# Performance work log

Measured on AMD Instinct MI355X. Metric: run time of the kernel, lower is better.

Reference implementation:

```python
import jax, jax.numpy as jnp
import numpy as np

INPUT_DIM = 1024
HIDDEN = [4096, 4096, 4096]
OUTPUT_DIM = 1024


def _cplx(a):
    # a: float32 array with leading axis 2 = (real, imag)
    return (a[0] + 1j * a[1]).astype(jnp.complex64)


def setup_inputs() -> dict:
    key = jax.random.key(0)
    ks = list(jax.random.split(key, 16))
    O = [INPUT_DIM] + HIDDEN[:-1] + [OUTPUT_DIM]  # O[0], O[1], O[2], O[3]
    I = HIDDEN  # I[1..3]
    inp = {"x": jax.random.normal(ks[0], (2, INPUT_DIM), dtype=jnp.float32)}
    for l in range(3):
        Il, Ol, Oprev = I[l], O[l + 1], O[l]
        w_std = 1.0 / np.sqrt(Il)
        c_std = 1.0 / np.sqrt(2 * Oprev)
        inp[f"W{l+1}"] = (jax.random.normal(ks[1 + 4 * l], (2, Ol, Il), dtype=jnp.float32) * w_std)
        inp[f"b{l+1}"] = jnp.zeros((2, Ol), dtype=jnp.float32)
        inp[f"G{l+1}"] = (jax.random.normal(ks[2 + 4 * l], (2, Il, Oprev), dtype=jnp.float32) * c_std)
        inp[f"s{l+1}"] = jnp.ones((Il,), dtype=jnp.float32)
    return inp


def _rbf_layer(y, W, b, G, s):
    # y: (O_prev,) complex; G: (I, O_prev) complex; W: (O, I); s: (I,) float
    diff = y[None, :] - G                                   # (I, O_prev)
    dist_sq = jnp.sum(diff.real ** 2 + diff.imag ** 2, axis=-1)  # (I,)
    phi = jnp.exp(-dist_sq / (2.0 * s))                     # (I,) real Gaussian kernel
    return W @ phi.astype(W.dtype) + b                      # (O,) complex


def reference(x, W1, b1, G1, s1, W2, b2, G2, s2, W3, b3, G3, s3):
    y = _cplx(x)
    for (W, b, G, s) in ((W1, b1, G1, s1), (W2, b2, G2, s2), (W3, b3, G3, s3)):
        y = _rbf_layer(y, _cplx(W), _cplx(b), _cplx(G), s)
    # return real/imag stacked as a real float32 array, shape (2, OUTPUT_DIM)
    return jnp.stack([y.real, y.imag]).astype(jnp.float32)
```

## Files before the change

### kernel.cpp

```cpp
#include <hip/hip_runtime.h>


#define D0 1024
#define H  4096

__device__ __forceinline__ float wave_sum(float v) {
#pragma unroll
    for (int off = 32; off > 0; off >>= 1) v += __shfl_down(v, off, 64);
    return v;
}

template <int COLS, int ROWS>
__global__ __launch_bounds__(256, 4) void phi_bpr(
        const float* __restrict__ G, const float* __restrict__ y2,
        const float* __restrict__ sv, float* __restrict__ phi) {
    const int lane = threadIdx.x & 63;
    const int w = threadIdx.x >> 6;
    const int row = blockIdx.x;
    constexpr int QL = COLS / 4;
    constexpr int NIT = QL / 256;
    constexpr int B = (NIT < 8) ? NIT : 8;

    const float* gre = G + (size_t)row * COLS + w * QL;
    const float* gim = gre + (size_t)ROWS * COLS;

    float acc = 0.f;
#pragma unroll
    for (int pl = 0; pl < 2; ++pl) {
        const float* gp = pl ? gim : gre;
        const float* yp = y2 + pl * COLS + w * QL;
#pragma unroll
        for (int it0 = 0; it0 < NIT; it0 += B) {
            float4 g[B], y[B];
#pragma unroll
            for (int u = 0; u < B; ++u) {
                const int j = lane * 4 + (it0 + u) * 256;
                g[u] = *(const float4*)(gp + j);
                y[u] = *(const float4*)(yp + j);
            }
#pragma unroll
            for (int u = 0; u < B; ++u) {
                float d;
                d = y[u].x - g[u].x; acc += d * d;
                d = y[u].y - g[u].y; acc += d * d;
                d = y[u].z - g[u].z; acc += d * d;
                d = y[u].w - g[u].w; acc += d * d;
            }
        }
    }
    acc = wave_sum(acc);
    __shared__ float sred[4];
    if (lane == 0) sred[w] = acc;
    __syncthreads();
    if (threadIdx.x == 0) {
        const float d = (sred[0] + sred[1]) + (sred[2] + sred[3]);
        phi[row] = expf(-d / (2.0f * sv[row]));
    }
}

template <int COLS, int ROWS>
__global__ __launch_bounds__(256, 4) void w_bpr(
        const float* __restrict__ W, const float* __restrict__ bias,
        const float* __restrict__ phi,
        float* __restrict__ ore, float* __restrict__ oim) {
    const int lane = threadIdx.x & 63;
    const int w = threadIdx.x >> 6;
    const int row = blockIdx.x;
    constexpr int QL = COLS / 4;
    constexpr int NIT = QL / 256;
    constexpr int B = (NIT < 8) ? NIT : 8;

    const float* wre = W + (size_t)row * COLS + w * QL;
    const float* wim = wre + (size_t)ROWS * COLS;
    const float* ph0 = phi + w * QL;

    float ac[2] = {0.f, 0.f};
#pragma unroll
    for (int pl = 0; pl < 2; ++pl) {
        const float* mp = pl ? wim : wre;
        float a = 0.f;
#pragma unroll
        for (int it0 = 0; it0 < NIT; it0 += B) {
            float4 m[B], p[B];
#pragma unroll
            for (int u = 0; u < B; ++u) {
                const int j = lane * 4 + (it0 + u) * 256;
                m[u] = *(const float4*)(mp + j);
                p[u] = *(const float4*)(ph0 + j);
            }
#pragma unroll
            for (int u = 0; u < B; ++u)
                a += m[u].x * p[u].x + m[u].y * p[u].y
                   + m[u].z * p[u].z + m[u].w * p[u].w;
        }
        ac[pl] = a;
    }
    const float ar = wave_sum(ac[0]);
    const float ai = wave_sum(ac[1]);
    __shared__ float sred[8];
    if (lane == 0) { sred[w] = ar; sred[4 + w] = ai; }
    __syncthreads();
    if (threadIdx.x == 0) {
        ore[row] = (sred[0] + sred[1]) + (sred[2] + sred[3]) + bias[row];
        oim[row] = (sred[4] + sred[5]) + (sred[6] + sred[7]) + bias[ROWS + row];
    }
}

extern "C" void kernel_launch(void* const* d_in, const int* in_sizes, int n_in,
                              void* d_out, int out_size, void* d_ws, size_t ws_size,
                              hipStream_t stream) {
    const float* x  = (const float*)d_in[0];
    const float* W1 = (const float*)d_in[1];
    const float* b1 = (const float*)d_in[2];
    const float* G1 = (const float*)d_in[3];
    const float* s1 = (const float*)d_in[4];
    const float* W2 = (const float*)d_in[5];
    const float* b2 = (const float*)d_in[6];
    const float* G2 = (const float*)d_in[7];
    const float* s2 = (const float*)d_in[8];
    const float* W3 = (const float*)d_in[9];
    const float* b3 = (const float*)d_in[10];
    const float* G3 = (const float*)d_in[11];
    const float* s3 = (const float*)d_in[12];
    float* out = (float*)d_out;

    float* ws  = (float*)d_ws;
    float* phi = ws;
    float* y2  = ws + H;

    phi_bpr<D0, H><<<H, 256, 0, stream>>>(G1, x, s1, phi);
    w_bpr<H, H><<<H, 256, 0, stream>>>(W1, b1, phi, y2, y2 + H);
    phi_bpr<H, H><<<H, 256, 0, stream>>>(G2, y2, s2, phi);
    w_bpr<H, H><<<H, 256, 0, stream>>>(W2, b2, phi, y2, y2 + H);
    phi_bpr<H, H><<<H, 256, 0, stream>>>(G3, y2, s3, phi);
    w_bpr<H, D0><<<D0, 256, 0, stream>>>(W3, b3, phi, out, out + D0);
}
```

Baseline: 112.1 us.

## Use persistent blocks with atomic work-stealing tickets for row-wise kernels

Result: slower. 324.9 us (+189.7%).

```diff
diff --git a/kernel.cpp b/kernel.cpp
--- a/kernel.cpp
+++ b/kernel.cpp
@@ -3,6 +3,7 @@
 
 #define D0 1024
 #define H  4096
+#define NPB 1024
 
 __device__ __forceinline__ float wave_sum(float v) {
 #pragma unroll
@@ -11,98 +12,153 @@
 }
 
 template <int COLS, int ROWS>
-__global__ __launch_bounds__(256, 4) void phi_bpr(
+__global__ __launch_bounds__(256, 4) void phi_tk(
         const float* __restrict__ G, const float* __restrict__ y2,
-        const float* __restrict__ sv, float* __restrict__ phi) {
+        const float* __restrict__ sv, float* __restrict__ phi,
+        int* __restrict__ tk) {
     const int lane = threadIdx.x & 63;
     const int w = threadIdx.x >> 6;
-    const int row = blockIdx.x;
-    constexpr int QL = COLS / 4;
-    constexpr int NIT = QL / 256;
-    constexpr int B = (NIT < 8) ? NIT : 8;
+    __shared__ int stk;
+    __shared__ float sred[4];
 
-    const float* gre = G + (size_t)row * COLS + w * QL;
-    const float* gim = gre + (size_t)ROWS * COLS;
-
-    float acc = 0.f;
+    if constexpr (COLS >= 4096) {
+        constexpr int QL = COLS / 4;
+        constexpr int NIT = QL / 256;
+        constexpr int B = 4;
+        for (;;) {
+            if (threadIdx.x == 0) stk = atomicAdd(tk, 1);
+            __syncthreads();
+            const int row = stk;
+            if (row >= ROWS) return;
+            const float* gre = G + (size_t)row * COLS + w * QL;
+            const float* gim = gre + (size_t)ROWS * COLS;
+            float acc = 0.f;
 #pragma unroll
-    for (int pl = 0; pl < 2; ++pl) {
-        const float* gp = pl ? gim : gre;
-        const float* yp = y2 + pl * COLS + w * QL;
+            for (int pl = 0; pl < 2; ++pl) {
+                const float* gp = pl ? gim : gre;
+                const float* yp = y2 + pl * COLS + w * QL;
 #pragma unroll
-        for (int it0 = 0; it0 < NIT; it0 += B) {
-            float4 g[B], y[B];
+                for (int it0 = 0; it0 < NIT; it0 += B) {
+                    float4 g[B], y[B];
 #pragma unroll
-            for (int u = 0; u < B; ++u) {
-                const int j = lane * 4 + (it0 + u) * 256;
-                g[u] = *(const float4*)(gp + j);
-                y[u] = *(const float4*)(yp + j);
+                    for (int u = 0; u < B; ++u) {
+                        const int j = lane * 4 + (it0 + u) * 256;
+                        g[u] = *(const float4*)(gp + j);
+                        y[u] = *(const float4*)(yp + j);
+                    }
+#pragma unroll
+                    for (int u = 0; u < B; ++u) {
+                        float d;
+                        d = y[u].x - g[u].x; acc += d * d;
+                        d = y[u].y - g[u].y; acc += d * d;
+                        d = y[u].z - g[u].z; acc += d * d;
+                        d = y[u].w - g[u].w; acc += d * d;
+                    }
+                }
             }
+            acc = wave_sum(acc);
+            if (lane == 0) sred[w] = acc;
+            __syncthreads();
+            if (threadIdx.x == 0) {
+                const float d = (sred[0] + sred[1]) + (sred[2] + sred[3]);
+                phi[row] = expf(-d / (2.0f * sv[row]));
+            }
+            __syncthreads();
+        }
+    } else {
+        constexpr int NIT = COLS / 256;
+        constexpr int B = 4;
+        for (;;) {
+            if (threadIdx.x == 0) stk = atomicAdd(tk, 1);
+            __syncthreads();
+            const int t = stk;
+            __syncthreads();
+            if (t * 4 >= ROWS) return;
+            const int row = t * 4 + w;
+            const float* gre = G + (size_t)row * COLS;
+            const float* gim = gre + (size_t)ROWS * COLS;
+            float acc = 0.f;
 #pragma unroll
-            for (int u = 0; u < B; ++u) {
-                float d;
-                d = y[u].x - g[u].x; acc += d * d;
-                d = y[u].y - g[u].y; acc += d * d;
-                d = y[u].z - g[u].z; acc += d * d;
-                d = y[u].w - g[u].w; acc += d * d;
+            for (int pl = 0; pl < 2; ++pl) {
+                const float* gp = pl ? gim : gre;
+                const float* yp = y2 + pl * COLS;
+#pragma unroll
+                for (int it0 = 0; it0 < NIT; it0 += B) {
+                    float4 g[B], y[B];
+#pragma unroll
+                    for (int u = 0; u < B; ++u) {
+                        const int j = lane * 4 + (it0 + u) * 256;
+                        g[u] = *(const float4*)(gp + j);
+                        y[u] = *(const float4*)(yp + j);
+                    }
+#pragma unroll
+                    for (int u = 0; u < B; ++u) {
+                        float d;
+                        d = y[u].x - g[u].x; acc += d * d;
+                        d = y[u].y - g[u].y; acc += d * d;
+                        d = y[u].z - g[u].z; acc += d * d;
+                        d = y[u].w - g[u].w; acc += d * d;
+                    }
+                }
             }
+            acc = wave_sum(acc);
+            if (lane == 0) phi[row] = expf(-acc / (2.0f * sv[row]));
         }
-    }
-    acc = wave_sum(acc);
-    __shared__ float sred[4];
-    if (lane == 0) sred[w] = acc;
-    __syncthreads();
-    if (threadIdx.x == 0) {
-        const float d = (sred[0] + sred[1]) + (sred[2] + sred[3]);
-        phi[row] = expf(-d / (2.0f * sv[row]));
     }
 }
 
 template <int COLS, int ROWS>
-__global__ __launch_bounds__(256, 4) void w_bpr(
+__global__ __launch_bounds__(256, 4) void w_tk(
         const float* __restrict__ W, const float* __restrict__ bias,
         const float* __restrict__ phi,
-        float* __restrict__ ore, float* __restrict__ oim) {
+        float* __restrict__ ore, float* __restrict__ oim,
+        int* __restrict__ tk) {
     const int lane = threadIdx.x & 63;
     const int w = threadIdx.x >> 6;
-    const int row = blockIdx.x;
     constexpr int QL = COLS / 4;
     constexpr int NIT = QL / 256;
-    constexpr int B = (NIT < 8) ? NIT : 8;
+    constexpr int B = 4;
+    __shared__ int stk;
+    __shared__ float sred[8];
 
-    const float* wre = W + (size_t)row * COLS + w * QL;
-    const float* wim = wre + (size_t)ROWS * COLS;
-    const float* ph0 = phi + w * QL;
-
-    float ac[2] = {0.f, 0.f};
+    for (;;) {
+        if (threadIdx.x == 0) stk = atomicAdd(tk, 1);
+        __syncthreads();
+        const int row = stk;
+        if (row >= ROWS) return;
+        const float* wre = W + (size_t)row * COLS + w * QL;
+        const float* wim = wre + (size_t)ROWS * COLS;
+        const float* ph0 = phi + w * QL;
+        float ac[2] = {0.f, 0.f};
 #pragma unroll
-    for (int pl = 0; pl < 2; ++pl) {
-        const float* mp = pl ? wim : wre;
-        float a = 0.f;
+        for (int pl = 0; pl < 2; ++pl) {
+            const float* mp = pl ? wim : wre;
+            float a = 0.f;
 #pragma unroll
-        for (int it0 = 0; it0 < NIT; it0 += B) {
-            float4 m[B], p[B];
+            for (int it0 = 0; it0 < NIT; it0 += B) {
+                float4 m[B], p[B];
 #pragma unroll
-            for (int u = 0; u < B; ++u) {
-                const int j = lane * 4 + (it0 + u) * 256;
-                m[u] = *(const float4*)(mp + j);
-                p[u] = *(const float4*)(ph0 + j);
+                for (int u = 0; u < B; ++u) {
+                    const int j = lane * 4 + (it0 + u) * 256;
+                    m[u] = *(const float4*)(mp + j);
+                    p[u] = *(const float4*)(ph0 + j);
+                }
+#pragma unroll
+                for (int u = 0; u < B; ++u)
+                    a += m[u].x * p[u].x + m[u].y * p[u].y
+                       + m[u].z * p[u].z + m[u].w * p[u].w;
             }
-#pragma unroll
-            for (int u = 0; u < B; ++u)
-                a += m[u].x * p[u].x + m[u].y * p[u].y
-                   + m[u].z * p[u].z + m[u].w * p[u].w;
+            ac[pl] = a;
         }
-        ac[pl] = a;
-    }
-    const float ar = wave_sum(ac[0]);
-    const float ai = wave_sum(ac[1]);
-    __shared__ float sred[8];
-    if (lane == 0) { sred[w] = ar; sred[4 + w] = ai; }
-    __syncthreads();
-    if (threadIdx.x == 0) {
-        ore[row] = (sred[0] + sred[1]) + (sred[2] + sred[3]) + bias[row];
-        oim[row] = (sred[4] + sred[5]) + (sred[6] + sred[7]) + bias[ROWS + row];
+        const float ar = wave_sum(ac[0]);
+        const float ai = wave_sum(ac[1]);
+        if (lane == 0) { sred[w] = ar; sred[4 + w] = ai; }
+        __syncthreads();
+        if (threadIdx.x == 0) {
+            ore[row] = (sred[0] + sred[1]) + (sred[2] + sred[3]) + bias[row];
+            oim[row] = (sred[4] + sred[5]) + (sred[6] + sred[7]) + bias[ROWS + row];
+        }
+        __syncthreads();
     }
 }
 
@@ -127,11 +183,14 @@
     float* ws  = (float*)d_ws;
     float* phi = ws;
     float* y2  = ws + H;
+    int* tk = (int*)(ws + 16384);
 
-    phi_bpr<D0, H><<<H, 256, 0, stream>>>(G1, x, s1, phi);
-    w_bpr<H, H><<<H, 256, 0, stream>>>(W1, b1, phi, y2, y2 + H);
-    phi_bpr<H, H><<<H, 256, 0, stream>>>(G2, y2, s2, phi);
-    w_bpr<H, H><<<H, 256, 0, stream>>>(W2, b2, phi, y2, y2 + H);
-    phi_bpr<H, H><<<H, 256, 0, stream>>>(G3, y2, s3, phi);
-    w_bpr<H, D0><<<D0, 256, 0, stream>>>(W3, b3, phi, out, out + D0);
+    hipMemsetAsync(tk, 0, 6 * 16 * sizeof(int), stream);
+
+    phi_tk<D0, H><<<NPB, 256, 0, stream>>>(G1, x, s1, phi, tk);
+    w_tk<H, H><<<NPB, 256, 0, stream>>>(W1, b1, phi, y2, y2 + H, tk + 16);
+    phi_tk<H, H><<<NPB, 256, 0, stream>>>(G2, y2, s2, phi, tk + 32);
+    w_tk<H, H><<<NPB, 256, 0, stream>>>(W2, b2, phi, y2, y2 + H, tk + 48);
+    phi_tk<H, H><<<NPB, 256, 0, stream>>>(G3, y2, s3, phi, tk + 64);
+    w_tk<H, D0><<<NPB, 256, 0, stream>>>(W3, b3, phi, out, out + D0, tk + 80);
 }
```
